# Kernel optimization log

Measured on AMD Instinct MI355X. Metric: run time of the kernel, lower is better.

## Reference

```python
import jax, jax.numpy as jnp
import numpy as np

D_MODEL = 2048
D_STATE = 64
D_CONV = 4
EXPAND = 2
HEADDIM = 64
NGROUPS = 1
CHUNK = 64
D_INNER = EXPAND * D_MODEL            # 4096
NHEADS = D_INNER // HEADDIM           # 64
D_XBC = D_INNER + 2 * NGROUPS * D_STATE
D_IN_PROJ = 2 * D_INNER + 2 * NGROUPS * D_STATE + NHEADS


def setup_inputs():
    key = jax.random.key(0)
    ks = jax.random.split(key, 8)
    B, L = 2, 4096
    u = jax.random.normal(ks[0], (B, L, D_MODEL), jnp.float32)
    W_in = jax.random.normal(ks[1], (D_IN_PROJ, D_MODEL), jnp.float32) * 0.02
    conv_w = jax.random.normal(ks[2], (D_XBC, D_CONV), jnp.float32) * 0.2
    conv_b = jnp.zeros((D_XBC,), jnp.float32)
    dt = jnp.exp(jax.random.uniform(ks[3], (NHEADS,)) * (np.log(0.1) - np.log(0.001)) + np.log(0.001))
    dt = jnp.clip(dt, 1e-4)
    dt_bias = dt + jnp.log(-jnp.expm1(-dt))
    A_log = jnp.log(jax.random.uniform(ks[4], (NHEADS,), minval=1.0, maxval=16.0))
    D_param = jnp.ones((NHEADS,), jnp.float32)
    norm_w = jnp.ones((D_INNER,), jnp.float32)
    W_out = jax.random.normal(ks[5], (D_MODEL, D_INNER), jnp.float32) * 0.02
    return dict(u=u, W_in=W_in, conv_w=conv_w, conv_b=conv_b, dt_bias=dt_bias,
                A_log=A_log, D_param=D_param, norm_w=norm_w, W_out=W_out)


def segsum(x):
    # x: (..., T) -> (..., T, T) with entry [l,s] = sum_{s< i <= l} x[i], -inf above diag
    T = x.shape[-1]
    mask_strict = jnp.tril(jnp.ones((T, T), bool), k=-1)
    mask_incl = jnp.tril(jnp.ones((T, T), bool), k=0)
    xe = jnp.where(mask_strict, x[..., :, None], 0.0)  # element [l,s] = x[l] if l>s
    xseg = jnp.cumsum(xe, axis=-2)
    return jnp.where(mask_incl, xseg, -jnp.inf)


def ssd_scan(X, A, Bm, Cm, block_len=CHUNK):
    # X: (b,L,h,p), A: (b,L,h), Bm/Cm: (b,L,h,n)
    b, seqlen, h, p = X.shape
    n = Bm.shape[-1]
    pad_len = (block_len - seqlen % block_len) % block_len
    if pad_len > 0:
        X = jnp.pad(X, ((0, 0), (0, pad_len), (0, 0), (0, 0)))
        A = jnp.pad(A, ((0, 0), (0, pad_len), (0, 0)))
        Bm = jnp.pad(Bm, ((0, 0), (0, pad_len), (0, 0), (0, 0)))
        Cm = jnp.pad(Cm, ((0, 0), (0, pad_len), (0, 0), (0, 0)))
    L = X.shape[1]
    c = L // block_len
    Xc = X.reshape(b, c, block_len, h, p)
    Ac = A.reshape(b, c, block_len, h).transpose(0, 3, 1, 2)  # (b,h,c,l)
    Bc = Bm.reshape(b, c, block_len, h, n)
    Cc = Cm.reshape(b, c, block_len, h, n)
    A_cum = jnp.cumsum(Ac, axis=-1)                           # (b,h,c,l)
    Lmat = jnp.exp(segsum(Ac))                                # (b,h,c,l,s)
    CB = jnp.einsum('bclhn,bcshn->bhcls', Cc, Bc)
    Y_diag = jnp.einsum('bhcls,bcshp->bhclp', CB * Lmat, Xc)
    decay_states = jnp.exp(A_cum[..., -1:] - A_cum)           # (b,h,c,l)
    states = jnp.einsum('bhcl,bclhn,bclhp->bhcpn', decay_states, Bc, Xc)
    init = jnp.zeros((b, h, 1, p, n), X.dtype)
    states = jnp.concatenate([init, states], axis=2)          # (b,h,c+1,p,n)
    chunk_decay = jnp.pad(A_cum[..., -1], ((0, 0), (0, 0), (1, 0)))  # (b,h,c+1)
    decay_chunk = jnp.exp(segsum(chunk_decay))                # (b,h,c+1,c+1)
    new_states = jnp.einsum('bhzc,bhcpn->bhzpn', decay_chunk, states)[:, :, :-1]
    Y_off = jnp.einsum('bclhn,bhcpn,bhcl->bhclp', Cc, new_states, jnp.exp(A_cum))
    Y = (Y_diag + Y_off).transpose(0, 2, 3, 1, 4).reshape(b, L, h, p)
    if pad_len > 0:
        Y = Y[:, :seqlen]
    return Y


def rmsnorm_grouped(x, w, ngroups, eps=1e-5):
    gs = x.shape[-1] // ngroups
    xg = x.reshape(*x.shape[:-1], ngroups, gs)
    xg = xg * jax.lax.rsqrt(jnp.mean(xg * xg, axis=-1, keepdims=True) + eps)
    return xg.reshape(x.shape) * w


def reference(u, W_in, conv_w, conv_b, dt_bias, A_log, D_param, norm_w, W_out):
    B, L, _ = u.shape
    zxbcdt = u @ W_in.T                                      # (B,L,d_in_proj)
    z = zxbcdt[..., :D_INNER]
    xBC = zxbcdt[..., D_INNER:D_INNER + D_XBC]
    dt = zxbcdt[..., D_INNER + D_XBC:]
    # causal depthwise conv1d, kernel D_CONV, left-pad D_CONV-1
    xpad = jnp.pad(xBC, ((0, 0), (D_CONV - 1, 0), (0, 0)))
    conv = conv_b
    for k in range(D_CONV):
        conv = conv + conv_w[:, k] * xpad[:, k:k + L, :]
    xBC = jax.nn.silu(conv)
    x = xBC[..., :D_INNER].reshape(B, L, NHEADS, HEADDIM)
    B_ssm = xBC[..., D_INNER:D_INNER + NGROUPS * D_STATE].reshape(B, L, NGROUPS, D_STATE)
    C_ssm = xBC[..., D_INNER + NGROUPS * D_STATE:].reshape(B, L, NGROUPS, D_STATE)
    if NGROUPS < NHEADS:
        rep = NHEADS // NGROUPS
        B_ssm = jnp.repeat(B_ssm, rep, axis=2)
        C_ssm = jnp.repeat(C_ssm, rep, axis=2)
    dt = jax.nn.softplus(dt + dt_bias)                        # (B,L,nheads)
    A = -jnp.exp(A_log)                                       # (nheads,)
    y = ssd_scan(x * dt[..., None], A * dt, B_ssm, C_ssm, block_len=CHUNK)
    y = y + D_param[:, None] * x
    y = y.reshape(B, L, D_INNER)
    y = rmsnorm_grouped(y * jax.nn.silu(z), norm_w, NGROUPS)
    return y @ W_out.T
```

## Files before the change

kernel.cpp:

```cpp
#include <hip/hip_runtime.h>
#include <hip/hip_bf16.h>
#include <math.h>

#define SEQ       4096
#define DMODEL    2048
#define DINNER    4096
#define DXBC      4224
#define NPROJ     8384
#define NHEADS    64
#define HDIM      64
#define DSTATE    64
#define NCHUNK    64
#define XLD       4352

typedef __attribute__((ext_vector_type(8))) _Float16 half8;
typedef __attribute__((ext_vector_type(4))) float floatx4;

__device__ __forceinline__ void async_copy16(void* lds, const void* g) {
  __builtin_amdgcn_global_load_lds(
      (const __attribute__((address_space(1))) unsigned int*)g,
      (__attribute__((address_space(3))) unsigned int*)lds, 16, 0, 0);
}

__device__ __forceinline__ float silu_f(float x) { return x / (1.f + expf(-x)); }

__global__ void diag_kernel(float* out, float v) { out[0] = v; }

__global__ void cvt_kernel(const float* __restrict__ src, _Float16* __restrict__ dst, int n) {
  int i = blockIdx.x * 256 + threadIdx.x;
  if (i < n) dst[i] = (_Float16)src[i];
}

__global__ void cvt_pad_kernel(const float* __restrict__ src, _Float16* __restrict__ dst) {
  int i = blockIdx.x * 256 + threadIdx.x;
  if (i >= 8448 * DMODEL) return;
  int r = i / DMODEL;
  dst[i] = (r < NPROJ) ? (_Float16)src[i] : (_Float16)0.f;
}

template <typename OT>
__global__ __launch_bounds__(256) void gemm_bt64(
    const _Float16* __restrict__ A, const _Float16* __restrict__ B,
    OT* __restrict__ C0, OT* __restrict__ C1, int K,
    int ldc0, int ldc1, int ncol0, int tiles_m, int tiles_n) {
  __shared__ __align__(16) _Float16 As[128 * 64];
  __shared__ __align__(16) _Float16 Bs[128 * 64];
  int t = threadIdx.x;
  int nt = tiles_m * tiles_n;
  int id = blockIdx.x;
  int id2 = ((nt & 7) == 0) ? ((id & 7) * (nt >> 3) + (id >> 3)) : id;
  int wband = tiles_m << 2;
  int g = id2 / wband;
  int rm = id2 - g * wband;
  int bw = tiles_n - (g << 2); if (bw > 4) bw = 4;
  int pn = (g << 2) + rm % bw;
  int pm = rm / bw;
  int m0 = pm * 128, n0 = pn * 128;

  int w = t >> 6, lane = t & 63, q = lane >> 4, r = lane & 15;
  int wm = (w >> 1) * 64, wn = (w & 1) * 64;
  int rowoff = lane >> 3;
  int chunkoff = ((lane & 7) ^ rowoff) * 8;
  const _Float16* gA[4];
  const _Float16* gB[4];
#pragma unroll
  for (int i = 0; i < 4; ++i) {
    gA[i] = A + (size_t)(m0 + i * 32 + w * 8 + rowoff) * K + chunkoff;
    gB[i] = B + (size_t)(n0 + i * 32 + w * 8 + rowoff) * K + chunkoff;
  }
  floatx4 acc[4][4] = {};
  for (int k0 = 0; k0 < K; k0 += 64) {
#pragma unroll
    for (int i = 0; i < 4; ++i) {
      async_copy16(As + (i * 32 + w * 8) * 64, gA[i] + k0);
      async_copy16(Bs + (i * 32 + w * 8) * 64, gB[i] + k0);
    }
    __syncthreads();
#pragma unroll
    for (int kk = 0; kk < 64; kk += 32) {
      half8 af[4], bf[4];
#pragma unroll
      for (int im = 0; im < 4; ++im) {
        int R = wm + im * 16 + r;
        af[im] = *(const half8*)&As[R * 64 + ((((kk >> 3) + q) ^ (R & 7)) << 3)];
      }
#pragma unroll
      for (int in = 0; in < 4; ++in) {
        int R = wn + in * 16 + r;
        bf[in] = *(const half8*)&Bs[R * 64 + ((((kk >> 3) + q) ^ (R & 7)) << 3)];
      }
#pragma unroll
      for (int im = 0; im < 4; ++im)
#pragma unroll
        for (int in = 0; in < 4; ++in)
          acc[im][in] =
              __builtin_amdgcn_mfma_f32_16x16x32_f16(af[im], bf[in], acc[im][in], 0, 0, 0);
    }
    __syncthreads();
  }
  OT* Cp = (n0 < ncol0) ? C0 : C1;
  int ldc = (n0 < ncol0) ? ldc0 : ldc1;
  int cb = (n0 < ncol0) ? n0 : n0 - ncol0;
#pragma unroll
  for (int im = 0; im < 4; ++im)
#pragma unroll
    for (int in = 0; in < 4; ++in)
#pragma unroll
      for (int i = 0; i < 4; ++i)
        Cp[(size_t)(m0 + wm + im * 16 + q * 4 + i) * ldc + cb + wn + in * 16 + r] =
            (OT)acc[im][in][i];
}

__global__ void conv_silu_kernel(const _Float16* __restrict__ xin, const float* __restrict__ conv_w,
                                 const float* __restrict__ conv_b, _Float16* __restrict__ xcv) {
  int idx = blockIdx.x * 256 + threadIdx.x;
  if (idx >= SEQ * DXBC) return;
  int l = idx / DXBC;
  int c = idx - l * DXBC;
  const _Float16* zc = xin + (size_t)l * XLD + c;
  float acc = conv_b[c];
#pragma unroll
  for (int k = 0; k < 4; ++k) {
    int off = k - 3;
    if (l + off >= 0) acc += conv_w[c * 4 + k] * (float)zc[(long)off * XLD];
  }
  xcv[idx] = (_Float16)silu_f(acc);
}

__global__ void dt_kernel(const _Float16* __restrict__ dtraw, const float* __restrict__ dt_bias,
                          const float* __restrict__ A_log, float* __restrict__ dtp,
                          float* __restrict__ dA) {
  int idx = blockIdx.x * 256 + threadIdx.x;
  if (idx >= SEQ * NHEADS) return;
  int h = idx & 63;
  int row = idx >> 6;
  float x = (float)dtraw[(size_t)row * XLD + h] + dt_bias[h];
  float dtv = (x > 20.f) ? x : log1pf(expf(x));
  dtp[idx] = dtv;
  dA[idx] = -expf(A_log[h]) * dtv;
}

__global__ void cumsum_kernel(const float* __restrict__ dA, float* __restrict__ acum,
                              float* __restrict__ chs) {
  int tid = blockIdx.x * 256 + threadIdx.x;
  if (tid >= NCHUNK * NHEADS) return;
  int h = tid & 63;
  int c = tid >> 6;
  int lbase = c * 64;
  float a = 0.f;
  for (int l = 0; l < 64; ++l) {
    a += dA[(size_t)(lbase + l) * 64 + h];
    acum[(size_t)tid * 64 + l] = a;
  }
  chs[tid] = a;
}

__global__ __launch_bounds__(256) void states_kernel(
    const _Float16* __restrict__ xcv, const float* __restrict__ dtp,
    const float* __restrict__ acum, const float* __restrict__ chs,
    _Float16* __restrict__ states) {
  int bid = blockIdx.x;
  int c = bid & 63, h = bid >> 6;
  int row0 = c * 64;
  int acbase = (c * 64 + h) * 64;
  __shared__ __align__(16) _Float16 XdT[64 * 72];
  __shared__ __align__(16) _Float16 BdT[64 * 72];
  __shared__ float dec[64];
  int t = threadIdx.x;
  if (t < 64) dec[t] = expf(chs[acbase >> 6] - acum[acbase + t]);
  __syncthreads();
#pragma unroll
  for (int i = 0; i < 16; ++i) {
    int flat = i * 256 + t;
    int l = flat >> 6, col = flat & 63;
    int grow = row0 + l;
    float dtv = dtp[(size_t)grow * 64 + h];
    float xv = (float)xcv[(size_t)grow * DXBC + h * 64 + col] * dtv;
    XdT[col * 72 + l] = (_Float16)xv;
    float bv = (float)xcv[(size_t)grow * DXBC + DINNER + col] * dec[l];
    BdT[col * 72 + l] = (_Float16)bv;
  }
  __syncthreads();
  int w = t >> 6, lane = t & 63, q = lane >> 4, r = lane & 15;
#pragma unroll
  for (int in = 0; in < 4; ++in) {
    floatx4 a4 = {0.f, 0.f, 0.f, 0.f};
#pragma unroll
    for (int k0 = 0; k0 < 64; k0 += 32) {
      half8 af = *(const half8*)&XdT[(w * 16 + r) * 72 + k0 + q * 8];
      half8 bf = *(const half8*)&BdT[(in * 16 + r) * 72 + k0 + q * 8];
      a4 = __builtin_amdgcn_mfma_f32_16x16x32_f16(af, bf, a4, 0, 0, 0);
    }
#pragma unroll
    for (int i = 0; i < 4; ++i)
      states[((size_t)bid * 64 + (w * 16 + q * 4 + i)) * 64 + in * 16 + r] = (_Float16)a4[i];
  }
}

__global__ __launch_bounds__(256) void scan_kernel(_Float16* __restrict__ states,
                                                   const float* __restrict__ chs) {
  int bid = blockIdx.x;
  int h = bid >> 4, seg = bid & 15;
  int e = seg * 256 + threadIdx.x;
  float carry = 0.f;
  for (int c = 0; c < 64; ++c) {
    size_t idx = ((size_t)(h * 64 + c)) * 4096 + e;
    float s = (float)states[idx];
    states[idx] = (_Float16)carry;
    carry = carry * expf(chs[c * 64 + h]) + s;
  }
}

__global__ __launch_bounds__(256) void yout_kernel(
    const _Float16* __restrict__ xcv, const float* __restrict__ dtp,
    const float* __restrict__ acum, const _Float16* __restrict__ sin_,
    const float* __restrict__ Dp, _Float16* __restrict__ Y) {
  int bid = blockIdx.x;
  int c = bid & 63, h = bid >> 6;
  int row0 = c * 64;
  int acbase = (c * 64 + h) * 64;
  __shared__ __align__(16) _Float16 Cs[64 * 72];
  __shared__ __align__(16) _Float16 Bt[64 * 72];
  __shared__ __align__(16) _Float16 XdT[64 * 72];
  __shared__ __align__(16) _Float16 Ms[64 * 72];
  __shared__ float acs[64];
  int t = threadIdx.x;
  if (t < 64) acs[t] = acum[acbase + t];
#pragma unroll
  for (int i = 0; i < 16; ++i) {
    int flat = i * 256 + t;
    int l = flat >> 6, col = flat & 63;
    int grow = row0 + l;
    const _Float16* rp = xcv + (size_t)grow * DXBC;
    Cs[l * 72 + col] = rp[DINNER + DSTATE + col];
    Bt[l * 72 + col] = rp[DINNER + col];
    float xv = (float)rp[h * 64 + col] * dtp[(size_t)grow * 64 + h];
    XdT[col * 72 + l] = (_Float16)xv;
  }
  __syncthreads();
  int w = t >> 6, lane = t & 63, q = lane >> 4, r = lane & 15;
  int m = w * 16 + r;
#pragma unroll
  for (int in = 0; in < 4; ++in) {
    floatx4 cb = {0.f, 0.f, 0.f, 0.f};
#pragma unroll
    for (int k0 = 0; k0 < 64; k0 += 32) {
      half8 af = *(const half8*)&Cs[m * 72 + k0 + q * 8];
      half8 bf = *(const half8*)&Bt[(in * 16 + r) * 72 + k0 + q * 8];
      cb = __builtin_amdgcn_mfma_f32_16x16x32_f16(af, bf, cb, 0, 0, 0);
    }
#pragma unroll
    for (int i = 0; i < 4; ++i) {
      int l = w * 16 + q * 4 + i;
      int s = in * 16 + r;
      float v = (s <= l) ? cb[i] * expf(acs[l] - acs[s]) : 0.f;
      Ms[l * 72 + s] = (_Float16)v;
    }
  }
  __syncthreads();
  size_t sbase = (size_t)bid * 4096;
  float Dh = Dp[h];
#pragma unroll
  for (int in = 0; in < 4; ++in) {
    floatx4 acc = {0.f, 0.f, 0.f, 0.f};
#pragma unroll
    for (int k0 = 0; k0 < 64; k0 += 32) {
      half8 af = *(const half8*)&Cs[m * 72 + k0 + q * 8];
      half8 bf = *(const half8*)&sin_[sbase + (size_t)(in * 16 + r) * 64 + k0 + q * 8];
      acc = __builtin_amdgcn_mfma_f32_16x16x32_f16(af, bf, acc, 0, 0, 0);
    }
#pragma unroll
    for (int i = 0; i < 4; ++i) acc[i] *= expf(acs[w * 16 + q * 4 + i]);
#pragma unroll
    for (int k0 = 0; k0 < 64; k0 += 32) {
      half8 af = *(const half8*)&Ms[m * 72 + k0 + q * 8];
      half8 bf = *(const half8*)&XdT[(in * 16 + r) * 72 + k0 + q * 8];
      acc = __builtin_amdgcn_mfma_f32_16x16x32_f16(af, bf, acc, 0, 0, 0);
    }
#pragma unroll
    for (int i = 0; i < 4; ++i) {
      int l = w * 16 + q * 4 + i;
      int p = in * 16 + r;
      int grow = row0 + l;
      float xv = (float)xcv[(size_t)grow * DXBC + h * 64 + p];
      Y[(size_t)grow * DINNER + h * 64 + p] = (_Float16)(acc[i] + Dh * xv);
    }
  }
}

__global__ __launch_bounds__(256) void rmsnorm_kernel(const _Float16* __restrict__ Y,
                                                      _Float16* __restrict__ Z,
                                                      const float* __restrict__ norm_w) {
  int row = blockIdx.x;
  const _Float16* y = Y + (size_t)row * DINNER;
  _Float16* z = Z + (size_t)row * DINNER;
  __shared__ float gbuf[DINNER];
  __shared__ float red[4];
  int t = threadIdx.x;
  float ss = 0.f;
#pragma unroll
  for (int i = 0; i < 16; ++i) {
    int j = i * 256 + t;
    float zv = (float)z[j];
    float g = (float)y[j] * silu_f(zv);
    gbuf[j] = g;
    ss += g * g;
  }
#pragma unroll
  for (int o = 32; o > 0; o >>= 1) ss += __shfl_down(ss, o, 64);
  if ((t & 63) == 0) red[t >> 6] = ss;
  __syncthreads();
  float rs = rsqrtf((red[0] + red[1] + red[2] + red[3]) / (float)DINNER + 1e-5f);
#pragma unroll
  for (int i = 0; i < 16; ++i) {
    int j = i * 256 + t;
    z[j] = (_Float16)(gbuf[j] * rs * norm_w[j]);
  }
}

extern "C" void kernel_launch(void* const* d_in, const int* in_sizes, int n_in,
                              void* d_out, int out_size, void* d_ws, size_t ws_size,
                              hipStream_t stream) {
  const float* u       = (const float*)d_in[0];
  const float* W_in    = (const float*)d_in[1];
  const float* conv_w  = (const float*)d_in[2];
  const float* conv_b  = (const float*)d_in[3];
  const float* dt_bias = (const float*)d_in[4];
  const float* A_log   = (const float*)d_in[5];
  const float* D_param = (const float*)d_in[6];
  const float* norm_w  = (const float*)d_in[7];
  const float* W_out   = (const float*)d_in[8];
  float* out = (float*)d_out;
  char* ws = (char*)d_ws;

  const size_t off_z      = 0;
  const size_t off_xbcdt  = 33554432ULL;
  const size_t off_Y      = 33554432ULL;
  const size_t off_xcv    = 69206016ULL;
  const size_t off_winbf  = 69206016ULL;
  const size_t off_states = 103809024ULL;
  const size_t off_ubf    = 103809024ULL;
  const size_t off_wout   = 103809024ULL;
  const size_t off_dtp    = 137363456ULL;
  const size_t off_dA     = 138412032ULL;
  const size_t off_acum   = 139460608ULL;
  const size_t off_chs    = 140509184ULL;
  const size_t ws_needed  = 140525568ULL;
  if (ws_size < ws_needed) {
    diag_kernel<<<1, 1, 0, stream>>>(out, (float)ws_size);
    return;
  }

  _Float16* zb     = (_Float16*)(ws + off_z);
  _Float16* xbcdtb = (_Float16*)(ws + off_xbcdt);
  _Float16* Yb     = (_Float16*)(ws + off_Y);
  _Float16* xcv    = (_Float16*)(ws + off_xcv);
  _Float16* winbf  = (_Float16*)(ws + off_winbf);
  _Float16* states = (_Float16*)(ws + off_states);
  _Float16* ubf    = (_Float16*)(ws + off_ubf);
  _Float16* woutbf = (_Float16*)(ws + off_wout);
  float*    dtp    = (float*)(ws + off_dtp);
  float*    dAb    = (float*)(ws + off_dA);
  float*    acum   = (float*)(ws + off_acum);
  float*    chs    = (float*)(ws + off_chs);

  for (int b = 0; b < 2; ++b) {
    const float* ub = u + (size_t)b * SEQ * DMODEL;
    float* outb = out + (size_t)b * SEQ * DMODEL;

    cvt_kernel<<<(SEQ * DMODEL + 255) / 256, 256, 0, stream>>>(ub, ubf, SEQ * DMODEL);
    cvt_pad_kernel<<<(8448 * DMODEL + 255) / 256, 256, 0, stream>>>(W_in, winbf);

    gemm_bt64<_Float16><<<32 * 66, 256, 0, stream>>>(
        ubf, winbf, zb, xbcdtb, DMODEL, DINNER, XLD, DINNER, 32, 66);

    conv_silu_kernel<<<(SEQ * DXBC + 255) / 256, 256, 0, stream>>>(xbcdtb, conv_w, conv_b, xcv);
    dt_kernel<<<(SEQ * NHEADS + 255) / 256, 256, 0, stream>>>(
        xbcdtb + DXBC, dt_bias, A_log, dtp, dAb);
    cumsum_kernel<<<(NCHUNK * NHEADS + 255) / 256, 256, 0, stream>>>(dAb, acum, chs);

    states_kernel<<<NHEADS * NCHUNK, 256, 0, stream>>>(xcv, dtp, acum, chs, states);
    scan_kernel<<<NHEADS * 16, 256, 0, stream>>>(states, chs);
    yout_kernel<<<NHEADS * NCHUNK, 256, 0, stream>>>(xcv, dtp, acum, states, D_param, Yb);

    rmsnorm_kernel<<<SEQ, 256, 0, stream>>>(Yb, zb, norm_w);

    cvt_kernel<<<(DMODEL * DINNER + 255) / 256, 256, 0, stream>>>(W_out, woutbf, DMODEL * DINNER);
    gemm_bt64<float><<<32 * 16, 256, 0, stream>>>(
        zb, woutbf, outb, outb, DINNER, DMODEL, DMODEL, 1 << 30, 32, 16);
  }
}
```

Measured before the change: 1.168 ms.

## Vectorize elementwise kernels, fuse dt/cumsum, use fast exp throughout

Merges the u and W_in fp32-to-fp16 conversions into one kernel and makes it and the W_out conversion process eight elements per thread with vector loads and stores. The conv+SiLU kernel now handles two channels per thread. The dt softplus and per-chunk cumsum are fused into one kernel through shared memory, which drops the dA buffer. RMSNorm keeps values in registers instead of shared memory and uses half8/float4 accesses. All expf calls become __expf, which trades a little accuracy for cheaper exponentials in the scan and output paths.

After: 1.163 ms. No clear change (-0.4%).

```diff
diff --git a/kernel.cpp b/kernel.cpp
--- a/kernel.cpp
+++ b/kernel.cpp
@@ -14,6 +14,7 @@
 #define XLD       4352
 
 typedef __attribute__((ext_vector_type(8))) _Float16 half8;
+typedef __attribute__((ext_vector_type(2))) _Float16 half2v;
 typedef __attribute__((ext_vector_type(4))) float floatx4;
 
 __device__ __forceinline__ void async_copy16(void* lds, const void* g) {
@@ -22,20 +23,41 @@
       (__attribute__((address_space(3))) unsigned int*)lds, 16, 0, 0);
 }
 
-__device__ __forceinline__ float silu_f(float x) { return x / (1.f + expf(-x)); }
+__device__ __forceinline__ float silu_f(float x) { return x / (1.f + __expf(-x)); }
+
+__device__ __forceinline__ void cvt8(const float* __restrict__ s, _Float16* __restrict__ d) {
+  float4 a = *(const float4*)s;
+  float4 b = *(const float4*)(s + 4);
+  half8 h;
+  h[0] = (_Float16)a.x; h[1] = (_Float16)a.y; h[2] = (_Float16)a.z; h[3] = (_Float16)a.w;
+  h[4] = (_Float16)b.x; h[5] = (_Float16)b.y; h[6] = (_Float16)b.z; h[7] = (_Float16)b.w;
+  *(half8*)d = h;
+}
 
 __global__ void diag_kernel(float* out, float v) { out[0] = v; }
 
-__global__ void cvt_kernel(const float* __restrict__ src, _Float16* __restrict__ dst, int n) {
+#define U_N8 (SEQ * DMODEL / 8)
+__global__ void cvt_in_kernel(const float* __restrict__ u, const float* __restrict__ W_in,
+                              _Float16* __restrict__ ubf, _Float16* __restrict__ winbf) {
   int i = blockIdx.x * 256 + threadIdx.x;
-  if (i < n) dst[i] = (_Float16)src[i];
-}
-
-__global__ void cvt_pad_kernel(const float* __restrict__ src, _Float16* __restrict__ dst) {
+  if (i < U_N8) {
+    cvt8(u + (size_t)i * 8, ubf + (size_t)i * 8);
+  } else {
+    int j = i - U_N8;
+    int row = j >> 8;
+    size_t off = (size_t)j * 8;
+    if (row < NPROJ) {
+      cvt8(W_in + off, winbf + off);
+    } else {
+      half8 zz = {};
+      *(half8*)(winbf + off) = zz;
+    }
+  }
+}
+
+__global__ void cvt8_kernel(const float* __restrict__ src, _Float16* __restrict__ dst, int n8) {
   int i = blockIdx.x * 256 + threadIdx.x;
-  if (i >= 8448 * DMODEL) return;
-  int r = i / DMODEL;
-  dst[i] = (r < NPROJ) ? (_Float16)src[i] : (_Float16)0.f;
+  if (i < n8) cvt8(src + (size_t)i * 8, dst + (size_t)i * 8);
 }
 
 template <typename OT>
@@ -114,45 +136,54 @@
 __global__ void conv_silu_kernel(const _Float16* __restrict__ xin, const float* __restrict__ conv_w,
                                  const float* __restrict__ conv_b, _Float16* __restrict__ xcv) {
   int idx = blockIdx.x * 256 + threadIdx.x;
-  if (idx >= SEQ * DXBC) return;
-  int l = idx / DXBC;
-  int c = idx - l * DXBC;
+  int l = idx / (DXBC / 2);
+  int c = (idx - l * (DXBC / 2)) * 2;
   const _Float16* zc = xin + (size_t)l * XLD + c;
-  float acc = conv_b[c];
+  float a0 = conv_b[c], a1 = conv_b[c + 1];
 #pragma unroll
   for (int k = 0; k < 4; ++k) {
     int off = k - 3;
-    if (l + off >= 0) acc += conv_w[c * 4 + k] * (float)zc[(long)off * XLD];
-  }
-  xcv[idx] = (_Float16)silu_f(acc);
-}
-
-__global__ void dt_kernel(const _Float16* __restrict__ dtraw, const float* __restrict__ dt_bias,
-                          const float* __restrict__ A_log, float* __restrict__ dtp,
-                          float* __restrict__ dA) {
-  int idx = blockIdx.x * 256 + threadIdx.x;
-  if (idx >= SEQ * NHEADS) return;
-  int h = idx & 63;
-  int row = idx >> 6;
-  float x = (float)dtraw[(size_t)row * XLD + h] + dt_bias[h];
-  float dtv = (x > 20.f) ? x : log1pf(expf(x));
-  dtp[idx] = dtv;
-  dA[idx] = -expf(A_log[h]) * dtv;
-}
-
-__global__ void cumsum_kernel(const float* __restrict__ dA, float* __restrict__ acum,
-                              float* __restrict__ chs) {
-  int tid = blockIdx.x * 256 + threadIdx.x;
-  if (tid >= NCHUNK * NHEADS) return;
-  int h = tid & 63;
-  int c = tid >> 6;
-  int lbase = c * 64;
-  float a = 0.f;
-  for (int l = 0; l < 64; ++l) {
-    a += dA[(size_t)(lbase + l) * 64 + h];
-    acum[(size_t)tid * 64 + l] = a;
-  }
-  chs[tid] = a;
+    if (l + off >= 0) {
+      half2v v = *(const half2v*)(zc + (long)off * XLD);
+      a0 += conv_w[c * 4 + k] * (float)v[0];
+      a1 += conv_w[c * 4 + 4 + k] * (float)v[1];
+    }
+  }
+  half2v o;
+  o[0] = (_Float16)silu_f(a0);
+  o[1] = (_Float16)silu_f(a1);
+  *(half2v*)(xcv + (size_t)l * DXBC + c) = o;
+}
+
+__global__ __launch_bounds__(256) void dtscan_kernel(
+    const _Float16* __restrict__ dtraw, const float* __restrict__ dt_bias,
+    const float* __restrict__ A_log, float* __restrict__ dtp,
+    float* __restrict__ acum, float* __restrict__ chs) {
+  int c = blockIdx.x;
+  __shared__ float dAs[64 * 65];
+  int t = threadIdx.x;
+  int h = t & 63;
+  float bias = dt_bias[h];
+  float negA = -__expf(A_log[h]);
+#pragma unroll
+  for (int i = 0; i < 16; ++i) {
+    int l = i * 4 + (t >> 6);
+    int row = c * 64 + l;
+    float x = (float)dtraw[(size_t)row * XLD + h] + bias;
+    float dtv = (x > 20.f) ? x : log1pf(__expf(x));
+    dtp[(size_t)row * 64 + h] = dtv;
+    dAs[l * 65 + h] = negA * dtv;
+  }
+  __syncthreads();
+  if (t < 64) {
+    float a = 0.f;
+    size_t base = ((size_t)c * 64 + t) * 64;
+    for (int l = 0; l < 64; ++l) {
+      a += dAs[l * 65 + t];
+      acum[base + l] = a;
+    }
+    chs[c * 64 + t] = a;
+  }
 }
 
 __global__ __launch_bounds__(256) void states_kernel(
@@ -167,7 +198,7 @@
   __shared__ __align__(16) _Float16 BdT[64 * 72];
   __shared__ float dec[64];
   int t = threadIdx.x;
-  if (t < 64) dec[t] = expf(chs[acbase >> 6] - acum[acbase + t]);
+  if (t < 64) dec[t] = __expf(chs[acbase >> 6] - acum[acbase + t]);
   __syncthreads();
 #pragma unroll
   for (int i = 0; i < 16; ++i) {
@@ -203,11 +234,12 @@
   int h = bid >> 4, seg = bid & 15;
   int e = seg * 256 + threadIdx.x;
   float carry = 0.f;
+#pragma unroll 2
   for (int c = 0; c < 64; ++c) {
     size_t idx = ((size_t)(h * 64 + c)) * 4096 + e;
     float s = (float)states[idx];
     states[idx] = (_Float16)carry;
-    carry = carry * expf(chs[c * 64 + h]) + s;
+    carry = carry * __expf(chs[c * 64 + h]) + s;
   }
 }
 
@@ -253,7 +285,7 @@
     for (int i = 0; i < 4; ++i) {
       int l = w * 16 + q * 4 + i;
       int s = in * 16 + r;
-      float v = (s <= l) ? cb[i] * expf(acs[l] - acs[s]) : 0.f;
+      float v = (s <= l) ? cb[i] * __expf(acs[l] - acs[s]) : 0.f;
       Ms[l * 72 + s] = (_Float16)v;
     }
   }
@@ -270,7 +302,7 @@
       acc = __builtin_amdgcn_mfma_f32_16x16x32_f16(af, bf, acc, 0, 0, 0);
     }
 #pragma unroll
-    for (int i = 0; i < 4; ++i) acc[i] *= expf(acs[w * 16 + q * 4 + i]);
+    for (int i = 0; i < 4; ++i) acc[i] *= __expf(acs[w * 16 + q * 4 + i]);
 #pragma unroll
     for (int k0 = 0; k0 < 64; k0 += 32) {
       half8 af = *(const half8*)&Ms[m * 72 + k0 + q * 8];
@@ -292,19 +324,23 @@
                                                       _Float16* __restrict__ Z,
                                                       const float* __restrict__ norm_w) {
   int row = blockIdx.x;
-  const _Float16* y = Y + (size_t)row * DINNER;
-  _Float16* z = Z + (size_t)row * DINNER;
-  __shared__ float gbuf[DINNER];
+  const half8* y8 = (const half8*)(Y + (size_t)row * DINNER);
+  half8* z8 = (half8*)(Z + (size_t)row * DINNER);
   __shared__ float red[4];
   int t = threadIdx.x;
+  float g[16];
   float ss = 0.f;
 #pragma unroll
-  for (int i = 0; i < 16; ++i) {
+  for (int i = 0; i < 2; ++i) {
     int j = i * 256 + t;
-    float zv = (float)z[j];
-    float g = (float)y[j] * silu_f(zv);
-    gbuf[j] = g;
-    ss += g * g;
+    half8 yv = y8[j];
+    half8 zv = z8[j];
+#pragma unroll
+    for (int e = 0; e < 8; ++e) {
+      float gv = (float)yv[e] * silu_f((float)zv[e]);
+      g[i * 8 + e] = gv;
+      ss += gv * gv;
+    }
   }
 #pragma unroll
   for (int o = 32; o > 0; o >>= 1) ss += __shfl_down(ss, o, 64);
@@ -312,9 +348,20 @@
   __syncthreads();
   float rs = rsqrtf((red[0] + red[1] + red[2] + red[3]) / (float)DINNER + 1e-5f);
 #pragma unroll
-  for (int i = 0; i < 16; ++i) {
+  for (int i = 0; i < 2; ++i) {
     int j = i * 256 + t;
-    z[j] = (_Float16)(gbuf[j] * rs * norm_w[j]);
+    const float4* w4 = (const float4*)(norm_w + j * 8);
+    float4 wa = w4[0], wb = w4[1];
+    half8 o;
+    o[0] = (_Float16)(g[i * 8 + 0] * rs * wa.x);
+    o[1] = (_Float16)(g[i * 8 + 1] * rs * wa.y);
+    o[2] = (_Float16)(g[i * 8 + 2] * rs * wa.z);
+    o[3] = (_Float16)(g[i * 8 + 3] * rs * wa.w);
+    o[4] = (_Float16)(g[i * 8 + 4] * rs * wb.x);
+    o[5] = (_Float16)(g[i * 8 + 5] * rs * wb.y);
+    o[6] = (_Float16)(g[i * 8 + 6] * rs * wb.z);
+    o[7] = (_Float16)(g[i * 8 + 7] * rs * wb.w);
+    z8[j] = o;
   }
 }
 
@@ -342,7 +389,6 @@
   const size_t off_ubf    = 103809024ULL;
   const size_t off_wout   = 103809024ULL;
   const size_t off_dtp    = 137363456ULL;
-  const size_t off_dA     = 138412032ULL;
   const size_t off_acum   = 139460608ULL;
   const size_t off_chs    = 140509184ULL;
   const size_t ws_needed  = 140525568ULL;
@@ -360,7 +406,6 @@
   _Float16* ubf    = (_Float16*)(ws + off_ubf);
   _Float16* woutbf = (_Float16*)(ws + off_wout);
   float*    dtp    = (float*)(ws + off_dtp);
-  float*    dAb    = (float*)(ws + off_dA);
   float*    acum   = (float*)(ws + off_acum);
   float*    chs    = (float*)(ws + off_chs);
 
@@ -368,16 +413,13 @@
     const float* ub = u + (size_t)b * SEQ * DMODEL;
     float* outb = out + (size_t)b * SEQ * DMODEL;
 
-    cvt_kernel<<<(SEQ * DMODEL + 255) / 256, 256, 0, stream>>>(ub, ubf, SEQ * DMODEL);
-    cvt_pad_kernel<<<(8448 * DMODEL + 255) / 256, 256, 0, stream>>>(W_in, winbf);
+    cvt_in_kernel<<<U_N8 / 256 + 8448, 256, 0, stream>>>(ub, W_in, ubf, winbf);
 
     gemm_bt64<_Float16><<<32 * 66, 256, 0, stream>>>(
         ubf, winbf, zb, xbcdtb, DMODEL, DINNER, XLD, DINNER, 32, 66);
 
-    conv_silu_kernel<<<(SEQ * DXBC + 255) / 256, 256, 0, stream>>>(xbcdtb, conv_w, conv_b, xcv);
-    dt_kernel<<<(SEQ * NHEADS + 255) / 256, 256, 0, stream>>>(
-        xbcdtb + DXBC, dt_bias, A_log, dtp, dAb);
-    cumsum_kernel<<<(NCHUNK * NHEADS + 255) / 256, 256, 0, stream>>>(dAb, acum, chs);
+    conv_silu_kernel<<<SEQ * (DXBC / 2) / 256, 256, 0, stream>>>(xbcdtb, conv_w, conv_b, xcv);
+    dtscan_kernel<<<NCHUNK, 256, 0, stream>>>(xbcdtb + DXBC, dt_bias, A_log, dtp, acum, chs);
 
     states_kernel<<<NHEADS * NCHUNK, 256, 0, stream>>>(xcv, dtp, acum, chs, states);
     scan_kernel<<<NHEADS * 16, 256, 0, stream>>>(states, chs);
@@ -385,7 +427,8 @@
 
     rmsnorm_kernel<<<SEQ, 256, 0, stream>>>(Yb, zb, norm_w);
 
-    cvt_kernel<<<(DMODEL * DINNER + 255) / 256, 256, 0, stream>>>(W_out, woutbf, DMODEL * DINNER);
+    cvt8_kernel<<<(DMODEL * DINNER / 8 + 255) / 256, 256, 0, stream>>>(
+        W_out, woutbf, DMODEL * DINNER / 8);
     gemm_bt64<float><<<32 * 16, 256, 0, stream>>>(
         zb, woutbf, outb, outb, DINNER, DMODEL, DMODEL, 1 << 30, 32, 16);
   }
```
